# Kernel optimization log

Measured on AMD Instinct MI355X. Metric: run time of the kernel, lower is better.

## Reference

```python
import jax, jax.numpy as jnp
import numpy as np

B, N, D_IN, D_OUT, H = 8, 1024, 768, 768, 12
D_HEAD = D_OUT // H  # 64; per-head softmax scale is sqrt(D_HEAD)


def setup_inputs() -> dict:
    key = jax.random.key(0)
    kx, kq, kk, kv, kwo, kbo = jax.random.split(key, 6)
    s_in = 1.0 / np.sqrt(D_IN)
    s_out = 1.0 / np.sqrt(D_OUT)
    return {
        "x": jax.random.normal(kx, (B, N, D_IN), dtype=jnp.float32),
        # stacked per-head Linear weights, torch layout [out, in] -> [H, d_head, D_IN]
        "Wq": jax.random.uniform(kq, (H, D_HEAD, D_IN), jnp.float32, -s_in, s_in),
        "Wk": jax.random.uniform(kk, (H, D_HEAD, D_IN), jnp.float32, -s_in, s_in),
        "Wv": jax.random.uniform(kv, (H, D_HEAD, D_IN), jnp.float32, -s_in, s_in),
        "Wo": jax.random.uniform(kwo, (D_OUT, D_OUT), jnp.float32, -s_out, s_out),
        "bo": jax.random.uniform(kbo, (D_OUT,), jnp.float32, -s_out, s_out),
    }


def reference(x, Wq, Wk, Wv, Wo, bo):
    # Per-head projections, batched over heads: [B, H, N, d_head]
    q = jnp.einsum('bnd,hed->bhne', x, Wq)
    k = jnp.einsum('bnd,hed->bhne', x, Wk)
    v = jnp.einsum('bnd,hed->bhne', x, Wv)
    scale = 1.0 / np.sqrt(D_HEAD)
    scores = jnp.einsum('bhie,bhje->bhij', q, k) * scale  # [B, H, N, N]
    att = jax.nn.softmax(scores, axis=-1)
    out = jnp.einsum('bhij,bhje->bhie', att, v)  # [B, H, N, d_head]
    # concat heads along last dim: [B, N, H*d_head]
    out = out.transpose(0, 2, 1, 3).reshape(B, N, D_OUT)
    return out @ Wo.T + bo
```

## Files before the change

### kernel.cpp

```cpp
#include <hip/hip_runtime.h>
#include <hip/hip_bf16.h>


typedef unsigned short u16;
typedef __attribute__((ext_vector_type(8))) short bf8;
typedef __attribute__((ext_vector_type(4))) short bf4;
typedef __attribute__((ext_vector_type(4))) float f4;
typedef __attribute__((ext_vector_type(4))) unsigned short us4;

#define NB 8
#define NSEQ 1024
#define DMODEL 768
#define NHEAD 12
#define DHEAD 64

#define XELEMS   (NB * NSEQ * DMODEL)
#define WELEMS   (DMODEL * DMODEL)

__device__ __forceinline__ float b2f(u16 u) {
  union { unsigned int i; float f; } c; c.i = ((unsigned int)u) << 16; return c.f;
}
__device__ __forceinline__ u16 f2b(float f) {
  union { float f; unsigned int i; } c; c.f = f;
  unsigned int r = c.i + 0x7fffu + ((c.i >> 16) & 1u);
  return (u16)(r >> 16);
}
__device__ __forceinline__ void gl_lds16(const u16* g, u16* l) {
  __builtin_amdgcn_global_load_lds(
      (const __attribute__((address_space(1))) unsigned int*)g,
      (__attribute__((address_space(3))) unsigned int*)l, 16, 0, 0);
}

struct CvtArgs {
  const float* src[5];
  u16* dst[5];
};
#define G0 (XELEMS / 4)
#define GW (WELEMS / 4)
#define GTOT (G0 + 4 * GW)

__global__ __launch_bounds__(256) void cvt_kernel(CvtArgs a) {
  size_t g = (size_t)blockIdx.x * 256 + threadIdx.x;
  if (g >= GTOT) return;
  int t; size_t off;
  if (g < G0) { t = 0; off = g; }
  else { size_t r = g - G0; t = 1 + (int)(r / GW); off = r % GW; }
  f4 v = *(const f4*)(a.src[t] + off * 4);
  us4 o;
  o[0] = f2b(v[0]); o[1] = f2b(v[1]); o[2] = f2b(v[2]); o[3] = f2b(v[3]);
  *(us4*)(a.dst[t] + off * 4) = o;
}

__global__ __launch_bounds__(512, 2) void qkv_gemm(
    const u16* __restrict__ x, const u16* __restrict__ Wq,
    const u16* __restrict__ Wk, const u16* __restrict__ Wv,
    u16* __restrict__ q, u16* __restrict__ k, u16* __restrict__ vt)
{
  __shared__ __align__(16) u16 lA[3][256 * 64];
  __shared__ __align__(16) u16 lB[3][128 * 64];

  const int tid  = threadIdx.x;
  const int lane = tid & 63;
  const int w    = tid >> 6;
  const int wm4  = w >> 1;
  const int wn2  = w & 1;
  const int col  = lane & 15;
  const int quad = lane >> 4;

  const int bid = blockIdx.x;
  const int wg  = (bid & 7) * 72 + (bid >> 3);
  const int bm  = wg / 18;
  const int bn  = wg % 18;

  const int m0 = bm * 256;
  const int proj = bn / 6;
  const u16* Wsel = (proj == 0) ? Wq : (proj == 1 ? Wk : Wv);
  const int nrem0 = (bn % 6) * 128;

  const int srow8 = lane >> 3;
  const int sg    = (lane & 7) ^ srow8;

  const u16* gA = x    + (size_t)(m0    + w * 8 + srow8) * DMODEL + sg * 8;
  const u16* gB = Wsel + (size_t)(nrem0 + w * 8 + srow8) * DMODEL + sg * 8;

  f4 acc[4][4];
#pragma unroll
  for (int i = 0; i < 4; i++)
#pragma unroll
    for (int j = 0; j < 4; j++) acc[i][j] = (f4)0.0f;

#define QKV_STAGE(T, BUF)                                                      \
  do {                                                                         \
    const int kk_ = (T) * 64;                                                  \
    _Pragma("unroll")                                                          \
    for (int r_ = 0; r_ < 4; r_++)                                             \
      gl_lds16(gA + (size_t)r_ * 64 * DMODEL + kk_,                            \
               &lA[BUF][(r_ * 64 + w * 8) * 64]);                              \
    _Pragma("unroll")                                                          \
    for (int r_ = 0; r_ < 2; r_++)                                             \
      gl_lds16(gB + (size_t)r_ * 64 * DMODEL + kk_,                            \
               &lB[BUF][(r_ * 64 + w * 8) * 64]);                              \
  } while (0)

  QKV_STAGE(0, 0);
  QKV_STAGE(1, 1);

  for (int t = 0; t < 12; t++) {
    if (t < 11) { asm volatile("s_waitcnt vmcnt(6)" ::: "memory"); }
    else        { asm volatile("s_waitcnt vmcnt(0)" ::: "memory"); }
    __builtin_amdgcn_s_barrier();
    asm volatile("" ::: "memory");

    if (t < 10) QKV_STAGE(t + 2, (t + 2) % 3);

    const int buf = t % 3;
    bf8 af[4][2], bfr[4][2];
#pragma unroll
    for (int mt = 0; mt < 4; mt++) {
      const int row = wm4 * 64 + mt * 16 + col;
#pragma unroll
      for (int kt = 0; kt < 2; kt++)
        af[mt][kt] = *(const bf8*)&lA[buf][row * 64 + (((kt * 4 + quad) ^ (row & 7)) << 3)];
    }
#pragma unroll
    for (int nt = 0; nt < 4; nt++) {
      const int row = wn2 * 64 + nt * 16 + col;
#pragma unroll
      for (int kt = 0; kt < 2; kt++)
        bfr[nt][kt] = *(const bf8*)&lB[buf][row * 64 + (((kt * 4 + quad) ^ (row & 7)) << 3)];
    }

    __builtin_amdgcn_s_setprio(1);
#pragma unroll
    for (int mt = 0; mt < 4; mt++)
#pragma unroll
      for (int nt = 0; nt < 4; nt++)
#pragma unroll
        for (int kt = 0; kt < 2; kt++)
          acc[mt][nt] = __builtin_amdgcn_mfma_f32_16x16x32_bf16(af[mt][kt], bfr[nt][kt], acc[mt][nt], 0, 0, 0);
    __builtin_amdgcn_s_setprio(0);
  }
#undef QKV_STAGE

  const int mw0 = m0 + wm4 * 64, nw0 = nrem0 + wn2 * 64;
  if (proj == 2) {
#pragma unroll
    for (int mt = 0; mt < 4; mt++) {
#pragma unroll
      for (int nt = 0; nt < 4; nt++) {
        const int nc = nw0 + nt * 16 + col;
        const int h = nc >> 6, e = nc & 63;
        const int t0 = mw0 + mt * 16 + quad * 4;
        const int b = t0 >> 10, tok0 = t0 & 1023;
        us4 pk;
#pragma unroll
        for (int r = 0; r < 4; r++) pk[r] = f2b(acc[mt][nt][r]);
        *(us4*)(vt + ((size_t)(b * NHEAD + h) * DHEAD + e) * NSEQ + tok0) = pk;
      }
    }
  } else {
    u16* dst = (proj == 0) ? q : k;
#pragma unroll
    for (int mt = 0; mt < 4; mt++) {
#pragma unroll
      for (int nt = 0; nt < 4; nt++) {
        const int nc = nw0 + nt * 16 + col;
        const int h = nc >> 6, e = nc & 63;
#pragma unroll
        for (int r = 0; r < 4; r++) {
          const int t = mw0 + mt * 16 + quad * 4 + r;
          const int b = t >> 10, tok = t & 1023;
          dst[((size_t)(b * NHEAD + h) * NSEQ + tok) * DHEAD + e] = f2b(acc[mt][nt][r]);
        }
      }
    }
  }
}

__global__ __launch_bounds__(256, 3) void attn_kernel(
    const u16* __restrict__ q, const u16* __restrict__ k,
    const u16* __restrict__ vt, u16* __restrict__ attn)
{
  __shared__ __align__(16) u16 ldsK[2][64 * 64];
  __shared__ __align__(16) u16 ldsV[2][64 * 64];
  __shared__ __align__(16) u16 ldsP[4][16][72];

  const int tid  = threadIdx.x;
  const int lane = tid & 63;
  const int w    = tid >> 6;
  const int col  = lane & 15;
  const int quad = lane >> 4;

  const int idx = blockIdx.x;
  const int bh = idx % 96, qc = idx / 96;
  const int b = bh / 12, h = bh % 12;

  const size_t head = ((size_t)b * NHEAD + h) * NSEQ * DHEAD;
  const int q0 = qc * 128 + w * 32;

  const int srow8 = lane >> 3;
  const int sg    = (lane & 7) ^ srow8;

  bf8 onesf;
#pragma unroll
  for (int j = 0; j < 8; j++) onesf[j] = (short)0x3F80;

  bf8 qf[2][2];
#pragma unroll
  for (int mt = 0; mt < 2; mt++)
#pragma unroll
    for (int kt = 0; kt < 2; kt++) {
      const int row = q0 + mt * 16 + col;
      bf8 t = *(const bf8*)(q + head + (size_t)row * DHEAD + kt * 32 + quad * 8);
#pragma unroll
      for (int j = 0; j < 8; j++) t[j] = (short)f2b(b2f((u16)t[j]) * 0.125f);
      qf[mt][kt] = t;
    }

  f4 lacc[2];
  f4 o[2][4];
#pragma unroll
  for (int mt = 0; mt < 2; mt++) {
    lacc[mt] = (f4)0.0f;
#pragma unroll
    for (int et = 0; et < 4; et++) o[mt][et] = (f4)0.0f;
  }

#pragma unroll
  for (int i = 0; i < 2; i++) {
    const int li = w * 2 + i;
    gl_lds16(k  + head + (size_t)(li * 8 + srow8) * DHEAD + sg * 8, &ldsK[0][li * 512]);
    gl_lds16(vt + head + (size_t)(li * 8 + srow8) * NSEQ + sg * 8,  &ldsV[0][li * 512]);
  }

  for (int t = 0; t < NSEQ / 64; t++) {
    const int cur = t & 1;
    __syncthreads();
    if (t < NSEQ / 64 - 1) {
      const int kb2 = (t + 1) * 64;
#pragma unroll
      for (int i = 0; i < 2; i++) {
        const int li = w * 2 + i;
        gl_lds16(k  + head + (size_t)(kb2 + li * 8 + srow8) * DHEAD + sg * 8,
                 &ldsK[cur ^ 1][li * 512]);
        gl_lds16(vt + head + (size_t)(li * 8 + srow8) * NSEQ + kb2 + sg * 8,
                 &ldsV[cur ^ 1][li * 512]);
      }
    }

    f4 s[2][4];
#pragma unroll
    for (int mt = 0; mt < 2; mt++)
#pragma unroll
      for (int nt = 0; nt < 4; nt++) s[mt][nt] = (f4)0.0f;
#pragma unroll
    for (int kt = 0; kt < 2; kt++) {
      bf8 kf[4];
#pragma unroll
      for (int nt = 0; nt < 4; nt++) {
        const int row = nt * 16 + col;
        kf[nt] = *(const bf8*)&ldsK[cur][row * 64 + (((kt * 4 + quad) ^ (col & 7)) << 3)];
      }
#pragma unroll
      for (int mt = 0; mt < 2; mt++)
#pragma unroll
        for (int nt = 0; nt < 4; nt++)
          s[mt][nt] = __builtin_amdgcn_mfma_f32_16x16x32_bf16(qf[mt][kt], kf[nt], s[mt][nt], 0, 0, 0);
    }

#pragma unroll
    for (int mt = 0; mt < 2; mt++) {
#pragma unroll
      for (int nt = 0; nt < 4; nt++)
#pragma unroll
        for (int r = 0; r < 4; r++)
          ldsP[w][quad * 4 + r][nt * 16 + col] = f2b(__expf(s[mt][nt][r]));
#pragma unroll
      for (int kt2 = 0; kt2 < 2; kt2++) {
        bf8 pf, vf[4];
        {
          const u16* pp = &ldsP[w][col][kt2 * 32 + quad * 8];
          bf4 lo = *(const bf4*)pp;
          bf4 hi = *(const bf4*)(pp + 4);
          pf = bf8{lo[0], lo[1], lo[2], lo[3], hi[0], hi[1], hi[2], hi[3]};
        }
        lacc[mt] = __builtin_amdgcn_mfma_f32_16x16x32_bf16(pf, onesf, lacc[mt], 0, 0, 0);
#pragma unroll
        for (int et = 0; et < 4; et++) {
          const int row = et * 16 + col;
          vf[et] = *(const bf8*)&ldsV[cur][row * 64 + (((kt2 * 4 + quad) ^ (col & 7)) << 3)];
        }
#pragma unroll
        for (int et = 0; et < 4; et++)
          o[mt][et] = __builtin_amdgcn_mfma_f32_16x16x32_bf16(pf, vf[et], o[mt][et], 0, 0, 0);
      }
    }
  }

#pragma unroll
  for (int mt = 0; mt < 2; mt++)
#pragma unroll
    for (int r = 0; r < 4; r++) {
      const float inv = 1.0f / lacc[mt][r];
      const int token = q0 + mt * 16 + quad * 4 + r;
#pragma unroll
      for (int et = 0; et < 4; et++)
        attn[(size_t)(b * NSEQ + token) * DMODEL + h * DHEAD + et * 16 + col] =
            f2b(o[mt][et][r] * inv);
    }
}

__global__ __launch_bounds__(256, 4) void out_gemm(
    const u16* __restrict__ attn, const u16* __restrict__ Wo,
    const float* __restrict__ bo, float* __restrict__ out)
{
  __shared__ __align__(16) u16 lA[2][128 * 32];
  __shared__ __align__(16) u16 lB[2][128 * 32];

  const int tid  = threadIdx.x;
  const int lane = tid & 63;
  const int w    = tid >> 6;
  const int wm   = w >> 1, wn = w & 1;
  const int col  = lane & 15;
  const int quad = lane >> 4;
  const int bm = blockIdx.x;
  const int bn = blockIdx.y;

  const int m0 = bm * 128;
  const int n0 = bn * 128;

  const int srow = lane >> 2;
  const int sg   = (lane & 3) ^ ((srow >> 1) & 3);
  const u16* gA0 = attn + (size_t)(m0 + w * 32 + srow) * DMODEL + sg * 8;
  const u16* gB0 = Wo   + (size_t)(n0 + w * 32 + srow) * DMODEL + sg * 8;

  f4 acc[4][4];
#pragma unroll
  for (int i = 0; i < 4; i++)
#pragma unroll
    for (int j = 0; j < 4; j++) acc[i][j] = (f4)0.0f;

  gl_lds16(gA0, &lA[0][(w * 32) * 32]);
  gl_lds16(gA0 + (size_t)16 * DMODEL, &lA[0][(w * 32 + 16) * 32]);
  gl_lds16(gB0, &lB[0][(w * 32) * 32]);
  gl_lds16(gB0 + (size_t)16 * DMODEL, &lB[0][(w * 32 + 16) * 32]);

  for (int it = 0; it < 24; it++) {
    const int cur = it & 1;
    __syncthreads();
    if (it < 23) {
      const int kk = (it + 1) * 32;
      gl_lds16(gA0 + kk, &lA[cur ^ 1][(w * 32) * 32]);
      gl_lds16(gA0 + (size_t)16 * DMODEL + kk, &lA[cur ^ 1][(w * 32 + 16) * 32]);
      gl_lds16(gB0 + kk, &lB[cur ^ 1][(w * 32) * 32]);
      gl_lds16(gB0 + (size_t)16 * DMODEL + kk, &lB[cur ^ 1][(w * 32 + 16) * 32]);
    }

    bf8 af[4], bfr[4];
#pragma unroll
    for (int mt = 0; mt < 4; mt++) {
      const int row = wm * 64 + mt * 16 + col;
      af[mt] = *(const bf8*)&lA[cur][row * 32 + ((quad ^ ((row >> 1) & 3)) << 3)];
    }
#pragma unroll
    for (int nt = 0; nt < 4; nt++) {
      const int row = wn * 64 + nt * 16 + col;
      bfr[nt] = *(const bf8*)&lB[cur][row * 32 + ((quad ^ ((row >> 1) & 3)) << 3)];
    }
#pragma unroll
    for (int mt = 0; mt < 4; mt++)
#pragma unroll
      for (int nt = 0; nt < 4; nt++)
        acc[mt][nt] = __builtin_amdgcn_mfma_f32_16x16x32_bf16(af[mt], bfr[nt], acc[mt][nt], 0, 0, 0);
  }

  const int mw0 = m0 + wm * 64, nw0 = n0 + wn * 64;
#pragma unroll
  for (int mt = 0; mt < 4; mt++)
#pragma unroll
    for (int nt = 0; nt < 4; nt++) {
      const int n = nw0 + nt * 16 + col;
      const float bias = bo[n];
#pragma unroll
      for (int r = 0; r < 4; r++) {
        const int row = mw0 + mt * 16 + quad * 4 + r;
        out[(size_t)row * DMODEL + n] = acc[mt][nt][r] + bias;
      }
    }
}

extern "C" void kernel_launch(void* const* d_in, const int* in_sizes, int n_in,
                              void* d_out, int out_size, void* d_ws, size_t ws_size,
                              hipStream_t stream) {
  const float* x  = (const float*)d_in[0];
  const float* Wq = (const float*)d_in[1];
  const float* Wk = (const float*)d_in[2];
  const float* Wv = (const float*)d_in[3];
  const float* Wo = (const float*)d_in[4];
  const float* bo = (const float*)d_in[5];
  float* out = (float*)d_out;

  u16* xb   = (u16*)d_ws;
  u16* wqb  = xb  + XELEMS;
  u16* wkb  = wqb + WELEMS;
  u16* wvb  = wkb + WELEMS;
  u16* wob  = wvb + WELEMS;
  u16* q    = wob + WELEMS;
  u16* k    = q   + XELEMS;
  u16* vt   = k   + XELEMS;
  u16* attn = vt  + XELEMS;

  CvtArgs ca;
  ca.src[0] = x;  ca.src[1] = Wq;  ca.src[2] = Wk;  ca.src[3] = Wv;  ca.src[4] = Wo;
  ca.dst[0] = xb; ca.dst[1] = wqb; ca.dst[2] = wkb; ca.dst[3] = wvb; ca.dst[4] = wob;

  cvt_kernel<<<dim3((GTOT + 255) / 256), 256, 0, stream>>>(ca);
  qkv_gemm<<<dim3(576), 512, 0, stream>>>(xb, wqb, wkb, wvb, q, k, vt);
  attn_kernel<<<dim3(768), 256, 0, stream>>>(q, k, vt, attn);
  out_gemm<<<dim3(64, 6), 256, 0, stream>>>(attn, wob, bo, out);
}
```

Measured before the change: 198.6 us.

## Compute transposed scores so P is written to LDS as vector stores

```diff
diff --git a/kernel.cpp b/kernel.cpp
--- a/kernel.cpp
+++ b/kernel.cpp
@@ -3,6 +3,7 @@
 
 
 typedef unsigned short u16;
+typedef unsigned int u32;
 typedef __attribute__((ext_vector_type(8))) short bf8;
 typedef __attribute__((ext_vector_type(4))) short bf4;
 typedef __attribute__((ext_vector_type(4))) float f4;
@@ -183,7 +184,7 @@
 {
   __shared__ __align__(16) u16 ldsK[2][64 * 64];
   __shared__ __align__(16) u16 ldsV[2][64 * 64];
-  __shared__ __align__(16) u16 ldsP[4][16][72];
+  __shared__ __align__(16) u16 ldsP[4][32][72];
 
   const int tid  = threadIdx.x;
   const int lane = tid & 63;
@@ -207,14 +208,14 @@
 
   bf8 qf[2][2];
 #pragma unroll
-  for (int mt = 0; mt < 2; mt++)
+  for (int qt = 0; qt < 2; qt++)
 #pragma unroll
     for (int kt = 0; kt < 2; kt++) {
-      const int row = q0 + mt * 16 + col;
+      const int row = q0 + qt * 16 + col;
       bf8 t = *(const bf8*)(q + head + (size_t)row * DHEAD + kt * 32 + quad * 8);
 #pragma unroll
       for (int j = 0; j < 8; j++) t[j] = (short)f2b(b2f((u16)t[j]) * 0.125f);
-      qf[mt][kt] = t;
+      qf[qt][kt] = t;
     }
 
   f4 lacc[2];
@@ -248,51 +249,59 @@
       }
     }
 
-    f4 s[2][4];
-#pragma unroll
-    for (int mt = 0; mt < 2; mt++)
-#pragma unroll
-      for (int nt = 0; nt < 4; nt++) s[mt][nt] = (f4)0.0f;
+    f4 st[4][2];
+#pragma unroll
+    for (int kvt = 0; kvt < 4; kvt++)
+#pragma unroll
+      for (int qt = 0; qt < 2; qt++) st[kvt][qt] = (f4)0.0f;
 #pragma unroll
     for (int kt = 0; kt < 2; kt++) {
       bf8 kf[4];
 #pragma unroll
-      for (int nt = 0; nt < 4; nt++) {
-        const int row = nt * 16 + col;
-        kf[nt] = *(const bf8*)&ldsK[cur][row * 64 + (((kt * 4 + quad) ^ (col & 7)) << 3)];
-      }
-#pragma unroll
-      for (int mt = 0; mt < 2; mt++)
-#pragma unroll
-        for (int nt = 0; nt < 4; nt++)
-          s[mt][nt] = __builtin_amdgcn_mfma_f32_16x16x32_bf16(qf[mt][kt], kf[nt], s[mt][nt], 0, 0, 0);
-    }
-
-#pragma unroll
-    for (int mt = 0; mt < 2; mt++) {
-#pragma unroll
-      for (int nt = 0; nt < 4; nt++)
-#pragma unroll
-        for (int r = 0; r < 4; r++)
-          ldsP[w][quad * 4 + r][nt * 16 + col] = f2b(__expf(s[mt][nt][r]));
-#pragma unroll
-      for (int kt2 = 0; kt2 < 2; kt2++) {
-        bf8 pf, vf[4];
-        {
-          const u16* pp = &ldsP[w][col][kt2 * 32 + quad * 8];
-          bf4 lo = *(const bf4*)pp;
-          bf4 hi = *(const bf4*)(pp + 4);
-          pf = bf8{lo[0], lo[1], lo[2], lo[3], hi[0], hi[1], hi[2], hi[3]};
-        }
+      for (int kvt = 0; kvt < 4; kvt++) {
+        const int row = kvt * 16 + col;
+        kf[kvt] = *(const bf8*)&ldsK[cur][row * 64 + (((kt * 4 + quad) ^ (col & 7)) << 3)];
+      }
+      __builtin_amdgcn_s_setprio(1);
+#pragma unroll
+      for (int kvt = 0; kvt < 4; kvt++)
+#pragma unroll
+        for (int qt = 0; qt < 2; qt++)
+          st[kvt][qt] = __builtin_amdgcn_mfma_f32_16x16x32_bf16(kf[kvt], qf[qt][kt], st[kvt][qt], 0, 0, 0);
+      __builtin_amdgcn_s_setprio(0);
+    }
+
+#pragma unroll
+    for (int kvt = 0; kvt < 4; kvt++)
+#pragma unroll
+      for (int qt = 0; qt < 2; qt++) {
+        const f4 p = st[kvt][qt];
+        bf4 pw;
+        pw[0] = (short)f2b(__expf(p[0]));
+        pw[1] = (short)f2b(__expf(p[1]));
+        pw[2] = (short)f2b(__expf(p[2]));
+        pw[3] = (short)f2b(__expf(p[3]));
+        *(bf4*)&ldsP[w][qt * 16 + col][kvt * 16 + quad * 4] = pw;
+      }
+    asm volatile("" ::: "memory");
+
+#pragma unroll
+    for (int kt2 = 0; kt2 < 2; kt2++) {
+      bf8 vf[4];
+#pragma unroll
+      for (int et = 0; et < 4; et++) {
+        const int row = et * 16 + col;
+        vf[et] = *(const bf8*)&ldsV[cur][row * 64 + (((kt2 * 4 + quad) ^ (col & 7)) << 3)];
+      }
+#pragma unroll
+      for (int mt = 0; mt < 2; mt++) {
+        const bf8 pf = *(const bf8*)&ldsP[w][mt * 16 + col][kt2 * 32 + quad * 8];
+        __builtin_amdgcn_s_setprio(1);
         lacc[mt] = __builtin_amdgcn_mfma_f32_16x16x32_bf16(pf, onesf, lacc[mt], 0, 0, 0);
-#pragma unroll
-        for (int et = 0; et < 4; et++) {
-          const int row = et * 16 + col;
-          vf[et] = *(const bf8*)&ldsV[cur][row * 64 + (((kt2 * 4 + quad) ^ (col & 7)) << 3)];
-        }
 #pragma unroll
         for (int et = 0; et < 4; et++)
           o[mt][et] = __builtin_amdgcn_mfma_f32_16x16x32_bf16(pf, vf[et], o[mt][et], 0, 0, 0);
+        __builtin_amdgcn_s_setprio(0);
       }
     }
   }
```

New measurement: 188.5 us. 5.1% less time.
